# Optimization experiments

Hardware: AMD Instinct MI355X
Metric: run time of the kernel (lower is better)

Reference implementation:

```python
import jax, jax.numpy as jnp
import numpy as np

T, N, M = 16, 10000, 2048          # timesteps, total nodes, masked nodes per step
F_IN, F1, F2, H = 256, 256, 256, 256  # feats_per_node, layer_1, layer_2, lstm_feats


def setup_inputs() -> dict:
    key = jax.random.key(0)
    ks = jax.random.split(key, 9)
    A = jax.random.normal(ks[0], (T, M, M), jnp.float32) / np.float32(np.sqrt(M))
    node_feats = jax.random.normal(ks[1], (N, F_IN), jnp.float32)
    # unique sorted indices per timestep (scatter target must be duplicate-free)
    mask = jax.vmap(lambda k: jnp.sort(jax.random.permutation(k, N)[:M]))(
        jax.random.split(ks[2], T)).astype(jnp.int32)
    u = lambda k, sh, fan: jax.random.uniform(k, sh, jnp.float32, -1.0, 1.0) * (2.0 / np.sqrt(fan))
    w0 = u(ks[3], (F_IN, F1), F_IN)
    w1 = u(ks[4], (F1, F2), F1)
    s = 1.0 / np.sqrt(H)
    W_ih = jax.random.uniform(ks[5], (4 * H, F2), jnp.float32, -s, s)
    W_hh = jax.random.uniform(ks[6], (4 * H, H), jnp.float32, -s, s)
    b_ih = jax.random.uniform(ks[7], (4 * H,), jnp.float32, -s, s)
    b_hh = jax.random.uniform(ks[8], (4 * H,), jnp.float32, -s, s)
    return {"A": A, "node_feats": node_feats, "mask": mask, "w0": w0, "w1": w1,
            "W_ih": W_ih, "W_hh": W_hh, "b_ih": b_ih, "b_hh": b_hh}


def reference(A, node_feats, mask, w0, w1, W_ih, W_hh, b_ih, b_hh):
    def gcn_step(Ah, idx):
        # layer 0: x = X @ W0 ; x[idx] = act(Ahat @ x[idx])
        x = node_feats @ w0                               # [N, F1]
        x = x.at[idx].set(jax.nn.relu(Ah @ x[idx]))
        # layer 1
        x = x @ w1                                        # [N, F2]
        x = x.at[idx].set(jax.nn.relu(Ah @ x[idx]))
        return x

    seq = jax.vmap(gcn_step)(A, mask)                     # [T, N, F2]

    def lstm_step(carry, xt):
        h, c = carry
        z = xt @ W_ih.T + h @ W_hh.T + (b_ih + b_hh)      # [N, 4H]
        i, f, g, o = jnp.split(z, 4, axis=-1)             # torch gate order i,f,g,o
        c = jax.nn.sigmoid(f) * c + jax.nn.sigmoid(i) * jnp.tanh(g)
        h = jax.nn.sigmoid(o) * jnp.tanh(c)
        return (h, c), None

    h0 = jnp.zeros((N, H), seq.dtype)
    (h, _), _ = jax.lax.scan(lstm_step, (h0, h0), seq)
    return h                                              # out[-1] of single-layer LSTM
```

## Files before the change

kernel.cpp:

```cpp
#include <hip/hip_runtime.h>
#include <cstdint>
#include <cstddef>

#pragma clang diagnostic ignored "-Waddress-space-conversion"

constexpr int T  = 16;
constexpr int N  = 10000;
constexpr int M  = 2048;
constexpr int F  = 256;
constexpr int H  = 256;
constexpr int G4 = 1024;
constexpr int NP = 10112;

typedef _Float16 f16;
using half8  = __attribute__((ext_vector_type(8))) f16;
using half4  = __attribute__((ext_vector_type(4))) f16;
using f32x4  = __attribute__((ext_vector_type(4))) float;

typedef __attribute__((address_space(1))) const void gas_t;
typedef __attribute__((address_space(3))) void las_t;

__device__ __forceinline__ void gl_lds16(const f16* g, f16* l) {
    __builtin_amdgcn_global_load_lds((gas_t*)g, (las_t*)l, 16, 0, 0);
}

__device__ __forceinline__ float fast_tanh(float x) {
    const float ax = fabsf(x);
    const float e  = __expf(-2.f * ax);
    const float t  = (1.f - e) / (1.f + e);
    return copysignf(t, x);
}

template<bool AF32, bool RELU, int OMODE>
__global__ __launch_bounds__(256, 2)
void gemm16(const void* __restrict__ Ag, long long sA,
            const f16*  __restrict__ Bg, long long sB,
            void*       __restrict__ Cg, long long sC,
            int Kk, int Nn, int Mvalid, int ldct)
{
    __shared__ f16 Als[2][128 * 32];
    __shared__ f16 Bls[2][128 * 32];

    const int tid  = threadIdx.x;
    const int lane = tid & 63;
    const int w    = tid >> 6;
    const int wm   = w >> 1, wn = w & 1;
    const int m0   = blockIdx.y * 128, n0 = blockIdx.x * 128;
    const int z    = blockIdx.z;

    const f16* Bt = Bg + (size_t)z * sB;
    const int srow = lane >> 2;
    const int scol = (lane & 3) * 8;

    f32x4 acc[4][4] = {};

    auto stage = [&](int buf, int kt) {
        const int k0 = kt * 32;
        #pragma unroll
        for (int c = 0; c < 2; ++c) {
            const int brow = w * 32 + c * 16;
            gl_lds16(Bt + (size_t)(n0 + brow + srow) * Kk + k0 + scol,
                     &Bls[buf][brow * 32]);
        }
        if constexpr (AF32) {
            const float* Af = (const float*)Ag + (size_t)z * sA;
            #pragma unroll
            for (int p = 0; p < 4; ++p) {
                const int flat = p * 1024 + tid * 4;
                const int r = flat >> 5, cc = flat & 31;
                float4 v = *(const float4*)&Af[(size_t)(m0 + r) * Kk + k0 + cc];
                half4 hv = { (f16)v.x, (f16)v.y, (f16)v.z, (f16)v.w };
                *(half4*)&Als[buf][r * 32 + cc] = hv;
            }
        } else {
            const f16* Af = (const f16*)Ag + (size_t)z * sA;
            #pragma unroll
            for (int c = 0; c < 2; ++c) {
                const int arow = w * 32 + c * 16;
                gl_lds16(Af + (size_t)(m0 + arow + srow) * Kk + k0 + scol,
                         &Als[buf][arow * 32]);
            }
        }
    };

    const int nk = Kk >> 5;
    stage(0, 0);
    int cur = 0;
    const int fr = lane & 15, fg = lane >> 4;

    for (int kt = 0; kt < nk; ++kt) {
        __syncthreads();
        if (kt + 1 < nk) stage(cur ^ 1, kt + 1);

        half8 a[4], b[4];
        #pragma unroll
        for (int i = 0; i < 4; ++i)
            a[i] = *(const half8*)&Als[cur][(wm * 64 + i * 16 + fr) * 32 + fg * 8];
        #pragma unroll
        for (int j = 0; j < 4; ++j)
            b[j] = *(const half8*)&Bls[cur][(wn * 64 + j * 16 + fr) * 32 + fg * 8];
        #pragma unroll
        for (int i = 0; i < 4; ++i)
            #pragma unroll
            for (int j = 0; j < 4; ++j)
                acc[i][j] = __builtin_amdgcn_mfma_f32_16x16x32_f16(a[i], b[j], acc[i][j], 0, 0, 0);
        cur ^= 1;
    }

    #pragma unroll
    for (int i = 0; i < 4; ++i) {
        const int gmb = m0 + wm * 64 + i * 16 + fg * 4;
        #pragma unroll
        for (int j = 0; j < 4; ++j) {
            const int gn = n0 + wn * 64 + j * 16 + fr;
            f32x4 v = acc[i][j];
            if (RELU) {
                v[0] = fmaxf(v[0], 0.f); v[1] = fmaxf(v[1], 0.f);
                v[2] = fmaxf(v[2], 0.f); v[3] = fmaxf(v[3], 0.f);
            }
            if constexpr (OMODE == 1) {
                f16* Ch = (f16*)Cg + (size_t)z * sC;
                #pragma unroll
                for (int r = 0; r < 4; ++r)
                    if (gmb + r < Mvalid) Ch[(size_t)(gmb + r) * Nn + gn] = (f16)v[r];
            } else {
                f16* Ct = (f16*)Cg + (size_t)z * sC;
                half4 hv = { (f16)v[0], (f16)v[1], (f16)v[2], (f16)v[3] };
                if (gmb + 3 < Mvalid) *(half4*)&Ct[(size_t)gn * ldct + gmb] = hv;
            }
        }
    }
}

__global__ __launch_bounds__(256, 2)
void gemm_lstm(const f16* __restrict__ h16, const f16* __restrict__ Whh,
               const f16* __restrict__ U, const f16* __restrict__ V,
               const int* __restrict__ invt, const float* __restrict__ bsum,
               float* __restrict__ Cb, f16* __restrict__ h16_out,
               float* __restrict__ hout)
{
    __shared__ f16 Als[2][128 * 32];
    __shared__ f16 Bls[2][128 * 32];

    const int tid  = threadIdx.x;
    const int lane = tid & 63;
    const int w    = tid >> 6;
    const int wm   = w >> 1, wn = w & 1;
    const int m0   = blockIdx.y * 128, n0 = blockIdx.x * 128;

    const int srow = lane >> 2;
    const int scol = (lane & 3) * 8;

    f32x4 acc[4][4] = {};

    auto stage = [&](int buf, int kt) {
        const int k0 = kt * 32;
        #pragma unroll
        for (int c = 0; c < 2; ++c) {
            const int row = w * 32 + c * 16;
            gl_lds16(Whh + (size_t)(n0 + row + srow) * H + k0 + scol, &Bls[buf][row * 32]);
            gl_lds16(h16 + (size_t)(m0 + row + srow) * H + k0 + scol, &Als[buf][row * 32]);
        }
    };

    stage(0, 0);
    int cur = 0;
    const int fr = lane & 15, fg = lane >> 4;

    for (int kt = 0; kt < H / 32; ++kt) {
        __syncthreads();
        if (kt + 1 < H / 32) stage(cur ^ 1, kt + 1);
        half8 a[4], b[4];
        #pragma unroll
        for (int i = 0; i < 4; ++i)
            a[i] = *(const half8*)&Als[cur][(wm * 64 + i * 16 + fr) * 32 + fg * 8];
        #pragma unroll
        for (int j = 0; j < 4; ++j)
            b[j] = *(const half8*)&Bls[cur][(wn * 64 + j * 16 + fr) * 32 + fg * 8];
        #pragma unroll
        for (int i = 0; i < 4; ++i)
            #pragma unroll
            for (int j = 0; j < 4; ++j)
                acc[i][j] = __builtin_amdgcn_mfma_f32_16x16x32_f16(a[i], b[j], acc[i][j], 0, 0, 0);
        cur ^= 1;
    }

    const int u = ((n0 >> 6) + wn) * 16 + fr;
    const int colbase = n0 + wn * 64 + fr;
    const float b0 = bsum[colbase],      b1 = bsum[colbase + 16],
                b2 = bsum[colbase + 32], b3 = bsum[colbase + 48];
    auto sig = [](float x) { return 1.f / (1.f + __expf(-x)); };

    #pragma unroll
    for (int i = 0; i < 4; ++i) {
        const int nodeb = m0 + wm * 64 + i * 16 + fg * 4;
        #pragma unroll
        for (int r = 0; r < 4; ++r) {
            const int node = nodeb + r;
            if (node >= N) continue;
            const int p = invt[node];
            const f16* xb = (p >= 0) ? V + (size_t)p * G4 : U + (size_t)node * G4;
            const float zi = acc[i][0][r] + (float)xb[colbase]      + b0;
            const float zf = acc[i][1][r] + (float)xb[colbase + 16] + b1;
            const float zg = acc[i][2][r] + (float)xb[colbase + 32] + b2;
            const float zo = acc[i][3][r] + (float)xb[colbase + 48] + b3;
            const size_t ci = (size_t)node * H + u;
            const float c = sig(zf) * Cb[ci] + sig(zi) * fast_tanh(zg);
            Cb[ci] = c;
            const float hv = sig(zo) * fast_tanh(c);
            h16_out[ci] = (f16)hv;
            if (hout) hout[ci] = hv;
        }
    }
}

__global__ __launch_bounds__(256)
void gather_T(const f16* __restrict__ Y0h, const int* __restrict__ mask,
              f16* __restrict__ GT)
{
    __shared__ f16 tile[64][F + 8];
    const int t = blockIdx.y, p0 = blockIdx.x * 64;
    const int tid = threadIdx.x;
    const int pr = tid >> 2;
    const int fc = (tid & 3) * 8;

    const int row = mask[t * M + p0 + pr];
    const f16* src = Y0h + (size_t)row * F;
    #pragma unroll
    for (int it = 0; it < 8; ++it) {
        const int f = it * 32 + fc;
        *(half8*)&tile[pr][f] = *(const half8*)&src[f];
    }
    __syncthreads();

    f16* dst = GT + ((size_t)t * F + tid) * M + p0;
    #pragma unroll
    for (int pc = 0; pc < 64; pc += 8) {
        half8 v;
        #pragma unroll
        for (int r = 0; r < 8; ++r) v[r] = tile[pc + r][tid];
        *(half8*)&dst[pc] = v;
    }
}

__global__ void cvt_f16(const float* __restrict__ s, f16* __restrict__ d, long long n)
{
    long long base = ((long long)blockIdx.x * blockDim.x + threadIdx.x) * 4;
    if (base + 3 < n) {
        float4 v = *(const float4*)&s[base];
        half4 hv = { (f16)v.x, (f16)v.y, (f16)v.z, (f16)v.w };
        *(half4*)&d[base] = hv;
    } else {
        for (long long k = base; k < n; ++k) d[k] = (f16)s[k];
    }
}

__global__ __launch_bounds__(256)
void prep(const float* __restrict__ nf,   f16* __restrict__ nf16,
          const float* __restrict__ w0,   f16* __restrict__ w0T,
          const float* __restrict__ w1,   f16* __restrict__ w1T,
          const float* __restrict__ W_ih, f16* __restrict__ Wih16,
          const float* __restrict__ W_hh, f16* __restrict__ Whh16,
          const float* __restrict__ b_ih, const float* __restrict__ b_hh,
          float* __restrict__ bsum,
          const int* __restrict__ mask, int* __restrict__ inv,
          float* __restrict__ Cb, f16* __restrict__ h16)
{
    const int b = blockIdx.x, tid = threadIdx.x;
    if (b < 512) {
        const float* s = (b < 256) ? w0 : w1;
        f16* d = (b < 256) ? w0T : w1T;
        const int i = (b & 255) * 256 + tid;
        const int r = i % F, c = i / F;
        d[(size_t)c * F + r] = (f16)s[(size_t)r * F + c];
    } else if (b < 1024) {
        const float* s = (b < 768) ? W_ih : W_hh;
        f16* d = (b < 768) ? Wih16 : Whh16;
        const int pcol = ((b - 512) & 255) * 4 + (tid >> 6);
        const int c64 = pcol >> 6, within = pcol & 63, gate = within >> 4, r = within & 15;
        const int srow = gate * 256 + c64 * 16 + r;
        const int k = (tid & 63) * 4;
        float4 v = *(const float4*)&s[(size_t)srow * F + k];
        half4 hv = { (f16)v.x, (f16)v.y, (f16)v.z, (f16)v.w };
        *(half4*)&d[(size_t)pcol * F + k] = hv;
    } else if (b == 1024) {
        #pragma unroll
        for (int it = 0; it < 4; ++it) {
            const int pcol = it * 256 + tid;
            const int c64 = pcol >> 6, within = pcol & 63, gate = within >> 4, r = within & 15;
            const int srow = gate * 256 + c64 * 16 + r;
            bsum[pcol] = b_ih[srow] + b_hh[srow];
        }
    } else if (b < 1153) {
        const int i = (b - 1025) * 256 + tid;
        inv[(size_t)(i / M) * N + mask[i]] = i % M;
    } else if (b < 3653) {
        const long long base = ((long long)(b - 1153) * 256 + tid) * 4;
        float4 v = *(const float4*)&nf[base];
        half4 hv = { (f16)v.x, (f16)v.y, (f16)v.z, (f16)v.w };
        *(half4*)&nf16[base] = hv;
    } else if (b < 3667) {
        const int idx = (b - 3653) * 256 + tid;
        half8 z = {};
        *(half8*)&nf16[(size_t)N * F + (size_t)idx * 8] = z;
    } else if (b < 6167) {
        const long long base = ((long long)(b - 3667) * 256 + tid) * 4;
        *(float4*)&Cb[base] = make_float4(0.f, 0.f, 0.f, 0.f);
    } else {
        const long long idx = (long long)(b - 6167) * 256 + tid;
        half8 z = {};
        *(half8*)&h16[idx * 8] = z;
    }
}

extern "C" void kernel_launch(void* const* d_in, const int* in_sizes, int n_in,
                              void* d_out, int out_size, void* d_ws, size_t ws_size,
                              hipStream_t stream)
{
    const float* A_all = (const float*)d_in[0];
    const float* nf    = (const float*)d_in[1];
    const int*   mask  = (const int*)  d_in[2];
    const float* w0    = (const float*)d_in[3];
    const float* w1    = (const float*)d_in[4];
    const float* W_ih  = (const float*)d_in[5];
    const float* W_hh  = (const float*)d_in[6];
    const float* b_ih  = (const float*)d_in[7];
    const float* b_hh  = (const float*)d_in[8];
    float* h = (float*)d_out;

    char* wp = (char*)d_ws;
    auto alloc = [&](size_t bytes) { char* p = wp; wp += (bytes + 255) & ~(size_t)255; return p; };
    f16*   nf16  = (f16*)alloc((size_t)NP * F * 2);
    f16*   w0T   = (f16*)alloc((size_t)F * F * 2);
    f16*   w1T   = (f16*)alloc((size_t)F * F * 2);
    f16*   Wih16 = (f16*)alloc((size_t)G4 * F * 2);
    f16*   Whh16 = (f16*)alloc((size_t)G4 * H * 2);
    float* bsum  = (float*)alloc((size_t)G4 * 4);
    f16*   Y0h   = (f16*)alloc((size_t)NP * F * 2);
    f16*   Y1h   = (f16*)alloc((size_t)NP * F * 2);
    f16*   Uh    = (f16*)alloc((size_t)NP * G4 * 2);
    f16*   GT    = (f16*)alloc((size_t)T * F * M * 2);
    f16*   Z1b   = (f16*)alloc((size_t)T * M * F * 2);
    f16*   Z2T   = (f16*)alloc((size_t)T * F * M * 2);
    f16*   Z3b   = (f16*)alloc((size_t)T * M * F * 2);
    f16*   Vb    = (f16*)alloc((size_t)4 * M * G4 * 2);
    float* Cb    = (float*)alloc((size_t)N * H * 4);
    f16*   h16   = (f16*)alloc((size_t)NP * H * 2);
    int*   inv   = (int*)alloc((size_t)T * N * 4);

    const size_t a16_bytes = (size_t)T * M * M * 2;
    const size_t used      = (size_t)(wp - (char*)d_ws);
    const bool   useA16    = (used + a16_bytes) <= ws_size;
    f16* A16 = useA16 ? (f16*)alloc(a16_bytes) : nullptr;

    hipMemsetAsync(inv, 0xFF, (size_t)T * N * 4, stream);

    prep<<<7431, 256, 0, stream>>>(nf, nf16, w0, w0T, w1, w1T,
                                   W_ih, Wih16, W_hh, Whh16,
                                   b_ih, b_hh, bsum, mask, inv, Cb, h16);

    gemm16<false,false,1><<<dim3(F / 128,  NP / 128, 1), 256, 0, stream>>>(nf16, 0, w0T,   0, Y0h, 0, F, F,  NP, 0);
    gemm16<false,false,1><<<dim3(F / 128,  NP / 128, 1), 256, 0, stream>>>(Y0h,  0, w1T,   0, Y1h, 0, F, F,  NP, 0);
    gemm16<false,false,1><<<dim3(G4 / 128, NP / 128, 1), 256, 0, stream>>>(Y1h,  0, Wih16, 0, Uh,  0, F, G4, NP, 0);

    gather_T<<<dim3(M / 64, T), 256, 0, stream>>>(Y0h, mask, GT);

    const long long sAmm = (long long)M * M;
    const long long sFM  = (long long)F * M;
    const long long sMF  = (long long)M * F;

    if (useA16) {
        cvt_f16<<<(int)(((long long)T * M * M / 4 + 255) / 256), 256, 0, stream>>>(
            A_all, A16, (long long)T * M * M);
        gemm16<false,true, 1><<<dim3(2, 16, T), 256, 0, stream>>>(A16, sAmm, GT,  sFM, Z1b, sMF, M, F, M, 0);
        gemm16<false,false,2><<<dim3(2, 16, T), 256, 0, stream>>>(Z1b, sMF,  w1T, 0,   Z2T, sFM, F, F, M, M);
        gemm16<false,true, 1><<<dim3(2, 16, T), 256, 0, stream>>>(A16, sAmm, Z2T, sFM, Z3b, sMF, M, F, M, 0);
    } else {
        gemm16<true, true, 1><<<dim3(2, 16, T), 256, 0, stream>>>(A_all, sAmm, GT,  sFM, Z1b, sMF, M, F, M, 0);
        gemm16<false,false,2><<<dim3(2, 16, T), 256, 0, stream>>>(Z1b,  sMF,  w1T, 0,   Z2T, sFM, F, F, M, M);
        gemm16<true, true, 1><<<dim3(2, 16, T), 256, 0, stream>>>(A_all, sAmm, Z2T, sFM, Z3b, sMF, M, F, M, 0);
    }

    for (int t = 0; t < T; ++t) {
        if ((t & 3) == 0) {
            gemm16<false,false,1><<<dim3(G4 / 128, M / 128, 4), 256, 0, stream>>>(
                Z3b + (size_t)t * M * F, sMF, Wih16, 0, Vb, (long long)M * G4, F, G4, M, 0);
        }
        gemm_lstm<<<dim3(G4 / 128, NP / 128, 1), 256, 0, stream>>>(
            h16, Whh16, Uh, Vb + (size_t)(t & 3) * M * G4, inv + (size_t)t * N,
            bsum, Cb, h16, (t == T - 1) ? h : nullptr);
    }
}
```

Before: 748.6 us.

## Interleave LSTM gate columns in input projection and store cell state in fp16

The W_ih weight rows and the bias sum are reordered so that the four gates of each hidden unit sit next to each other. The LSTM epilogue can then fetch the input-projection contribution with one half4 load and the bias with one float4 load, instead of four strided scalar loads. The cell state buffer changes from fp32 to fp16, which halves its read/write traffic on every timestep and shrinks the prep zeroing. Keeping the cell state in fp16 loses precision as it accumulates across the 16 steps. The V buffer produced by the masked path must follow the same interleaved column layout for the results to stay correct.

```diff
diff --git a/kernel.cpp b/kernel.cpp
--- a/kernel.cpp
+++ b/kernel.cpp
@@ -136,7 +136,7 @@
 void gemm_lstm(const f16* __restrict__ h16, const f16* __restrict__ Whh,
                const f16* __restrict__ U, const f16* __restrict__ V,
                const int* __restrict__ invt, const float* __restrict__ bsum,
-               float* __restrict__ Cb, f16* __restrict__ h16_out,
+               f16* __restrict__ Cb, f16* __restrict__ h16_out,
                float* __restrict__ hout)
 {
     __shared__ f16 Als[2][128 * 32];
@@ -186,9 +186,7 @@
     }
 
     const int u = ((n0 >> 6) + wn) * 16 + fr;
-    const int colbase = n0 + wn * 64 + fr;
-    const float b0 = bsum[colbase],      b1 = bsum[colbase + 16],
-                b2 = bsum[colbase + 32], b3 = bsum[colbase + 48];
+    const float4 bv = *(const float4*)&bsum[u * 4];
     auto sig = [](float x) { return 1.f / (1.f + __expf(-x)); };
 
     #pragma unroll
@@ -200,13 +198,14 @@
             if (node >= N) continue;
             const int p = invt[node];
             const f16* xb = (p >= 0) ? V + (size_t)p * G4 : U + (size_t)node * G4;
-            const float zi = acc[i][0][r] + (float)xb[colbase]      + b0;
-            const float zf = acc[i][1][r] + (float)xb[colbase + 16] + b1;
-            const float zg = acc[i][2][r] + (float)xb[colbase + 32] + b2;
-            const float zo = acc[i][3][r] + (float)xb[colbase + 48] + b3;
+            const half4 xv = *(const half4*)&xb[u * 4];
+            const float zi = acc[i][0][r] + (float)xv[0] + bv.x;
+            const float zf = acc[i][1][r] + (float)xv[1] + bv.y;
+            const float zg = acc[i][2][r] + (float)xv[2] + bv.z;
+            const float zo = acc[i][3][r] + (float)xv[3] + bv.w;
             const size_t ci = (size_t)node * H + u;
-            const float c = sig(zf) * Cb[ci] + sig(zi) * fast_tanh(zg);
-            Cb[ci] = c;
+            const float c = sig(zf) * (float)Cb[ci] + sig(zi) * fast_tanh(zg);
+            Cb[ci] = (f16)c;
             const float hv = sig(zo) * fast_tanh(c);
             h16_out[ci] = (f16)hv;
             if (hout) hout[ci] = hv;
@@ -264,7 +263,7 @@
           const float* __restrict__ b_ih, const float* __restrict__ b_hh,
           float* __restrict__ bsum,
           const int* __restrict__ mask, int* __restrict__ inv,
-          float* __restrict__ Cb, f16* __restrict__ h16)
+          f16* __restrict__ Cb, f16* __restrict__ h16)
 {
     const int b = blockIdx.x, tid = threadIdx.x;
     if (b < 512) {
@@ -274,11 +273,18 @@
         const int r = i % F, c = i / F;
         d[(size_t)c * F + r] = (f16)s[(size_t)r * F + c];
     } else if (b < 1024) {
-        const float* s = (b < 768) ? W_ih : W_hh;
-        f16* d = (b < 768) ? Wih16 : Whh16;
+        const bool ih = (b < 768);
+        const float* s = ih ? W_ih : W_hh;
+        f16* d = ih ? Wih16 : Whh16;
         const int pcol = ((b - 512) & 255) * 4 + (tid >> 6);
-        const int c64 = pcol >> 6, within = pcol & 63, gate = within >> 4, r = within & 15;
-        const int srow = gate * 256 + c64 * 16 + r;
+        int srow;
+        if (ih) {
+            const int gate = pcol & 3, unit = pcol >> 2;
+            srow = gate * 256 + unit;
+        } else {
+            const int c64 = pcol >> 6, within = pcol & 63, gate = within >> 4, r = within & 15;
+            srow = gate * 256 + c64 * 16 + r;
+        }
         const int k = (tid & 63) * 4;
         float4 v = *(const float4*)&s[(size_t)srow * F + k];
         half4 hv = { (f16)v.x, (f16)v.y, (f16)v.z, (f16)v.w };
@@ -287,8 +293,8 @@
         #pragma unroll
         for (int it = 0; it < 4; ++it) {
             const int pcol = it * 256 + tid;
-            const int c64 = pcol >> 6, within = pcol & 63, gate = within >> 4, r = within & 15;
-            const int srow = gate * 256 + c64 * 16 + r;
+            const int gate = pcol & 3, unit = pcol >> 2;
+            const int srow = gate * 256 + unit;
             bsum[pcol] = b_ih[srow] + b_hh[srow];
         }
     } else if (b < 1153) {
@@ -303,11 +309,12 @@
         const int idx = (b - 3653) * 256 + tid;
         half8 z = {};
         *(half8*)&nf16[(size_t)N * F + (size_t)idx * 8] = z;
-    } else if (b < 6167) {
-        const long long base = ((long long)(b - 3667) * 256 + tid) * 4;
-        *(float4*)&Cb[base] = make_float4(0.f, 0.f, 0.f, 0.f);
+    } else if (b < 4917) {
+        const long long idx = (long long)(b - 3667) * 256 + tid;
+        half8 z = {};
+        *(half8*)&Cb[idx * 8] = z;
     } else {
-        const long long idx = (long long)(b - 6167) * 256 + tid;
+        const long long idx = (long long)(b - 4917) * 256 + tid;
         half8 z = {};
         *(half8*)&h16[idx * 8] = z;
     }
@@ -344,7 +351,7 @@
     f16*   Z2T   = (f16*)alloc((size_t)T * F * M * 2);
     f16*   Z3b   = (f16*)alloc((size_t)T * M * F * 2);
     f16*   Vb    = (f16*)alloc((size_t)4 * M * G4 * 2);
-    float* Cb    = (float*)alloc((size_t)N * H * 4);
+    f16*   Cb    = (f16*)alloc((size_t)N * H * 2);
     f16*   h16   = (f16*)alloc((size_t)NP * H * 2);
     int*   inv   = (int*)alloc((size_t)T * N * 4);
 
@@ -355,7 +362,7 @@
 
     hipMemsetAsync(inv, 0xFF, (size_t)T * N * 4, stream);
 
-    prep<<<7431, 256, 0, stream>>>(nf, nf16, w0, w0T, w1, w1T,
+    prep<<<6181, 256, 0, stream>>>(nf, nf16, w0, w0T, w1, w1T,
                                    W_ih, Wih16, W_hh, Whh16,
                                    b_ih, b_hh, bsum, mask, inv, Cb, h16);
 
```

New measurement: 756.0 us. Within noise of the previous version (+1.0%).
